# Optimization experiments

Hardware: AMD Instinct MI355X
Metric: run time of the kernel (lower is better)

The kernel has to match this reference:

```python
import jax, jax.numpy as jnp
import numpy as np

B, S, F = 32, 8, 4
N0, N1, N2 = 2048, 4096, 2048
H, OUT = 1024, 256
IN = N0 + N1 + N2  # 8192
SC_LAYERS = 2


def setup_inputs() -> dict:
    key = jax.random.key(0)
    ks = jax.random.split(key, 16)
    rn = jax.random.normal
    inp = {
        'xs0': rn(ks[0], (B, S, N0), jnp.float32),
        'xs1': rn(ks[1], (B, S, N1), jnp.float32),
        'xs2': rn(ks[2], (B, S, N2), jnp.float32),
        # dense Laplacians, scaled so L@x keeps unit-ish variance
        'L0': rn(ks[3], (N0, N0), jnp.float32) / np.sqrt(N0).astype(np.float32),
        'L1': rn(ks[4], (N1, N1), jnp.float32) / np.sqrt(N1).astype(np.float32),
        'L2': rn(ks[5], (N2, N2), jnp.float32) / np.sqrt(N2).astype(np.float32),
        # per-layer, per-filter diagonal weights (std=0.01 as in torch init)
        'Wc0': 0.01 * rn(ks[6], (SC_LAYERS, F, N0), jnp.float32),
        'Wc1': 0.01 * rn(ks[7], (SC_LAYERS, F, N1), jnp.float32),
        'Wc2': 0.01 * rn(ks[8], (SC_LAYERS, F, N2), jnp.float32),
        # MLP params (xavier-ish)
        'W_in': rn(ks[9], (IN, H), jnp.float32) / np.sqrt(IN).astype(np.float32),
        'b_in': jnp.zeros((H,), jnp.float32),
        'W_h': rn(ks[10], (H, H), jnp.float32) / np.sqrt(H).astype(np.float32),
        'b_h': jnp.zeros((H,), jnp.float32),
        'W_out': rn(ks[11], (H, OUT), jnp.float32) / np.sqrt(H).astype(np.float32),
        'b_out': jnp.zeros((OUT,), jnp.float32),
    }
    return inp


def _conv_stack(x, L, Wc):
    # x: [B, S, n]; L: [n, n]; Wc: [layers, F, n]
    for l in range(Wc.shape[0]):
        # batched Laplacian matmul: (L @ x_bs) for every (b, s)
        Lx = jnp.einsum('bsn,mn->bsm', x, L)  # [B, S, n]
        # diagonal filter scaling + activation + sum over filters (fused)
        x = jax.nn.relu(Lx[:, :, None, :] * Wc[l][None, None, :, :]).sum(axis=2)
    return x


def reference(xs0, xs1, xs2, L0, L1, L2, Wc0, Wc1, Wc2,
              W_in, b_in, W_h, b_h, W_out, b_out):
    h = jnp.concatenate([
        _conv_stack(xs0, L0, Wc0),
        _conv_stack(xs1, L1, Wc1),
        _conv_stack(xs2, L2, Wc2),
    ], axis=-1)                      # [B, S, IN]
    h = h.sum(axis=1)                # sum over sequence -> [B, IN]
    h = jax.nn.relu(h @ W_in + b_in)
    h = jax.nn.relu(h @ W_h + b_h)   # single hidden layer (nn_layers=2)
    return h @ W_out + b_out         # [B, OUT]
```

## Files before the change

kernel.cpp:

```cpp
#include <hip/hip_runtime.h>
#include <hip/hip_bf16.h>


#define B_    32
#define S_    8
#define BS_   256
#define F_    4
#define IN_   8192
#define H_    1024
#define OUT_  256

#define L_TOT  25165824LL
#define LOFF1  4194304LL
#define LOFF2  20971520LL

typedef __attribute__((ext_vector_type(8)))  short bf16x8;
typedef __attribute__((ext_vector_type(4)))  short short4v;
typedef __attribute__((ext_vector_type(16))) float f32x16;

typedef const __attribute__((address_space(1))) void* gas_ptr;
typedef __attribute__((address_space(3))) void* las_ptr;

__device__ __forceinline__ void gload16(const void* g, void* s) {
    __builtin_amdgcn_global_load_lds((gas_ptr)g, (las_ptr)s, 16, 0, 0);
}

__device__ __forceinline__ unsigned short rne_bf16(float f) {
    unsigned int u = __builtin_bit_cast(unsigned int, f);
    u += 0x7FFFu + ((u >> 16) & 1u);
    return (unsigned short)(u >> 16);
}

__global__ void k_prep(const float* __restrict__ Wc0, const float* __restrict__ Wc1,
                       const float* __restrict__ Wc2, float* __restrict__ PM) {
    int idx = blockIdx.x * 256 + threadIdx.x;
    if (idx >= 2 * IN_) return;
    int l = idx / IN_, n = idx % IN_;
    const float* Wc; int nb, j;
    if (n < 2048)      { Wc = Wc0; nb = 2048; j = n;        }
    else if (n < 6144) { Wc = Wc1; nb = 4096; j = n - 2048; }
    else               { Wc = Wc2; nb = 2048; j = n - 6144; }
    float p = 0.f, m = 0.f;
    #pragma unroll
    for (int f = 0; f < F_; ++f) {
        float w = Wc[(l * F_ + f) * nb + j];
        p += fmaxf(w, 0.f);
        m += fmaxf(-w, 0.f);
    }
    PM[(l * 2 + 0) * IN_ + n] = p;
    PM[(l * 2 + 1) * IN_ + n] = m;
}

__global__ void k_cvtL(const float* __restrict__ L0, const float* __restrict__ L1,
                       const float* __restrict__ L2, unsigned short* __restrict__ Lb) {
    const int gid = blockIdx.x * 256 + threadIdx.x;
    #pragma unroll 4
    for (int it = 0; it < 12; ++it) {
        long long e = ((long long)it * 524288 + gid) * 4;
        const float* src; long long off;
        if (e < LOFF1)      { src = L0; off = 0; }
        else if (e < LOFF2) { src = L1; off = LOFF1; }
        else                { src = L2; off = LOFF2; }
        float4 v = *(const float4*)(src + (e - off));
        short4v o;
        o.x = (short)rne_bf16(v.x); o.y = (short)rne_bf16(v.y);
        o.z = (short)rne_bf16(v.z); o.w = (short)rne_bf16(v.w);
        *(short4v*)(Lb + e) = o;
    }
}

__global__ void k_splitX(const float* __restrict__ x0, const float* __restrict__ x1,
                         const float* __restrict__ x2,
                         unsigned short* __restrict__ Xhi, unsigned short* __restrict__ Xlo) {
    int e = (blockIdx.x * 256 + threadIdx.x) * 4;
    int m = e >> 13, c = e & 8191;
    const float* src; int n, c0;
    if (c < 2048)      { src = x0; n = 2048; c0 = c; }
    else if (c < 6144) { src = x1; n = 4096; c0 = c - 2048; }
    else               { src = x2; n = 2048; c0 = c - 6144; }
    float4 v = *(const float4*)(src + (size_t)m * n + c0);
    float a[4] = {v.x, v.y, v.z, v.w};
    short hv[4], lv[4];
    #pragma unroll
    for (int i = 0; i < 4; ++i) {
        unsigned short hb = rne_bf16(a[i]);
        float hf = __builtin_bit_cast(float, (unsigned int)hb << 16);
        hv[i] = (short)hb;
        lv[i] = (short)rne_bf16(a[i] - hf);
    }
    short4v h = {hv[0], hv[1], hv[2], hv[3]};
    short4v l = {lv[0], lv[1], lv[2], lv[3]};
    *(short4v*)(Xhi + (size_t)m * IN_ + c) = h;
    *(short4v*)(Xlo + (size_t)m * IN_ + c) = l;
}

__global__ __launch_bounds__(256, 3) void k_gemm(
    const unsigned short* __restrict__ Xhi, const unsigned short* __restrict__ Xlo,
    const unsigned short* __restrict__ Lb,
    float* __restrict__ pf)
{
    __shared__ __attribute__((aligned(16))) unsigned short Ah[2][64 * 32];
    __shared__ __attribute__((aligned(16))) unsigned short Al[2][64 * 32];
    __shared__ __attribute__((aligned(16))) unsigned short Bs[2][128 * 32];

    const int bx = blockIdx.x;
    int n_, noff, mt, nt, sk; long long loff;
    if (bx < 128) {
        int u = bx; sk = u & 1; u >>= 1; mt = u >> 4; nt = u & 15;
        n_ = 2048; noff = 0; loff = 0;
    } else if (bx < 640) {
        int u = bx - 128; sk = u & 3; u >>= 2; mt = u >> 5; nt = u & 31;
        n_ = 4096; noff = 2048; loff = LOFF1;
    } else {
        int u = bx - 640; sk = u & 1; u >>= 1; mt = u >> 4; nt = u & 15;
        n_ = 2048; noff = 6144; loff = LOFF2;
    }
    const int k0 = sk << 10;

    const int tid = threadIdx.x, l = tid & 63, w = tid >> 6;

    const int sr  = 16 * w + (l >> 2);
    const int slg = (((l & 3) ^ ((l >> 3) & 3)) << 3);
    const unsigned short* gAh = Xhi + (size_t)(mt * 64 + sr) * IN_ + noff + k0 + slg;
    const unsigned short* gAl = Xlo + (size_t)(mt * 64 + sr) * IN_ + noff + k0 + slg;
    const unsigned short* gB0 = Lb + loff + (size_t)(nt * 128 + sr) * n_ + k0 + slg;
    const unsigned short* gB1 = Lb + loff + (size_t)(nt * 128 + 64 + sr) * n_ + k0 + slg;
    char* dAh[2] = {(char*)&Ah[0][0] + w * 1024, (char*)&Ah[1][0] + w * 1024};
    char* dAl[2] = {(char*)&Al[0][0] + w * 1024, (char*)&Al[1][0] + w * 1024};
    char* dB0[2] = {(char*)&Bs[0][0] + w * 1024, (char*)&Bs[1][0] + w * 1024};
    char* dB1[2] = {(char*)&Bs[0][0] + 4096 + w * 1024, (char*)&Bs[1][0] + 4096 + w * 1024};

    const int l31 = l & 31, lh = l >> 5;
    const int wm = w >> 1, wn = w & 1;
    const int ra  = (wm * 32 + l31) * 32;
    const int rb0 = (wn * 64 + l31) * 32;
    const int rb1 = rb0 + 32 * 32;
    const int swz = ((l31 >> 1) & 3);

    f32x16 acc0, acc1;
    #pragma unroll
    for (int r = 0; r < 16; ++r) { acc0[r] = 0.f; acc1[r] = 0.f; }

    gload16(gAh, dAh[0]); gload16(gAl, dAl[0]);
    gload16(gB0, dB0[0]); gload16(gB1, dB1[0]);
    __syncthreads();

    for (int it = 0; it < 32; ++it) {
        const int cur = it & 1, nxt = cur ^ 1;
        if (it + 1 < 32) {
            const int ko = (it + 1) * 32;
            gload16(gAh + ko, dAh[nxt]); gload16(gAl + ko, dAl[nxt]);
            gload16(gB0 + ko, dB0[nxt]); gload16(gB1 + ko, dB1[nxt]);
        }
        #pragma unroll
        for (int t = 0; t < 2; ++t) {
            const int sidx = (((2 * t + lh) ^ swz) << 3);
            bf16x8 fah = *(const bf16x8*)&Ah[cur][ra + sidx];
            bf16x8 fal = *(const bf16x8*)&Al[cur][ra + sidx];
            bf16x8 fb0 = *(const bf16x8*)&Bs[cur][rb0 + sidx];
            bf16x8 fb1 = *(const bf16x8*)&Bs[cur][rb1 + sidx];
            acc0 = __builtin_amdgcn_mfma_f32_32x32x16_bf16(fal, fb0, acc0, 0, 0, 0);
            acc0 = __builtin_amdgcn_mfma_f32_32x32x16_bf16(fah, fb0, acc0, 0, 0, 0);
            acc1 = __builtin_amdgcn_mfma_f32_32x32x16_bf16(fal, fb1, acc1, 0, 0, 0);
            acc1 = __builtin_amdgcn_mfma_f32_32x32x16_bf16(fah, fb1, acc1, 0, 0, 0);
        }
        __syncthreads();
    }

    const int colg = noff + nt * 128 + wn * 64 + l31;
    float* po = pf + ((size_t)sk * 256 + (size_t)mt * 64 + wm * 32 + 4 * lh) * IN_;
    #pragma unroll
    for (int r = 0; r < 16; ++r) {
        int row = (r & 3) + 8 * (r >> 2);
        po[(size_t)row * IN_ + colg]      = acc0[r];
        po[(size_t)row * IN_ + colg + 32] = acc1[r];
    }
}

__global__ void k_epi0(const float* __restrict__ pf,
                       const float* __restrict__ Pv, const float* __restrict__ Mv,
                       unsigned short* __restrict__ Yhi, unsigned short* __restrict__ Ylo) {
    int e = (blockIdx.x * 256 + threadIdx.x) * 4;
    int m = e >> 13, c = e & 8191;
    const int nsl = (c >= 2048 && c < 6144) ? 4 : 2;
    const float* p0 = pf + (size_t)m * IN_ + c;
    float vs[4] = {0.f, 0.f, 0.f, 0.f};
    for (int s = 0; s < nsl; ++s) {
        float4 v = *(const float4*)(p0 + (size_t)s * 256 * IN_);
        vs[0] += v.x; vs[1] += v.y; vs[2] += v.z; vs[3] += v.w;
    }
    float4 pv = *(const float4*)(Pv + c);
    float4 mv = *(const float4*)(Mv + c);
    float pa[4] = {pv.x, pv.y, pv.z, pv.w};
    float ma[4] = {mv.x, mv.y, mv.z, mv.w};
    short hv[4], lv[4];
    #pragma unroll
    for (int j = 0; j < 4; ++j) {
        float y = fmaxf(vs[j], 0.f) * pa[j] + fmaxf(-vs[j], 0.f) * ma[j];
        unsigned short hb = rne_bf16(y);
        float hf = __builtin_bit_cast(float, (unsigned int)hb << 16);
        hv[j] = (short)hb;
        lv[j] = (short)rne_bf16(y - hf);
    }
    short4v h = {hv[0], hv[1], hv[2], hv[3]};
    short4v lo = {lv[0], lv[1], lv[2], lv[3]};
    *(short4v*)(Yhi + (size_t)m * IN_ + c) = h;
    *(short4v*)(Ylo + (size_t)m * IN_ + c) = lo;
}

__global__ void k_epi1s(const float* __restrict__ pf,
                        const float* __restrict__ Pv, const float* __restrict__ Mv,
                        float* __restrict__ hsum) {
    int e = (blockIdx.x * 256 + threadIdx.x) * 4;
    int b = e >> 13, c = e & 8191;
    const int nsl = (c >= 2048 && c < 6144) ? 4 : 2;
    float4 pv = *(const float4*)(Pv + c);
    float4 mv = *(const float4*)(Mv + c);
    float pa[4] = {pv.x, pv.y, pv.z, pv.w};
    float ma[4] = {mv.x, mv.y, mv.z, mv.w};
    float hs[4] = {0.f, 0.f, 0.f, 0.f};
    for (int q = 0; q < 8; ++q) {
        const int m = b * 8 + q;
        const float* p0 = pf + (size_t)m * IN_ + c;
        float vs[4] = {0.f, 0.f, 0.f, 0.f};
        for (int s = 0; s < nsl; ++s) {
            float4 v = *(const float4*)(p0 + (size_t)s * 256 * IN_);
            vs[0] += v.x; vs[1] += v.y; vs[2] += v.z; vs[3] += v.w;
        }
        #pragma unroll
        for (int j = 0; j < 4; ++j)
            hs[j] += fmaxf(vs[j], 0.f) * pa[j] + fmaxf(-vs[j], 0.f) * ma[j];
    }
    *(float4*)(hsum + (size_t)b * IN_ + c) = *(float4*)hs;
}

template<int KC>
__global__ __launch_bounds__(256) void k_mlp3(
    const float* __restrict__ X, const float* __restrict__ W,
    float* __restrict__ P, int K, int H)
{
    __shared__ float Xs[32][KC];
    const int tid = threadIdx.x;
    const int lane = tid & 63;
    const int mg = tid >> 6;
    const int h = (blockIdx.x * 64 + lane) * 4;
    const int c = blockIdx.y, k0 = c * KC;

    for (int i = tid * 4; i < 32 * KC; i += 1024) {
        int m = i / KC, kk = i % KC;
        *(float4*)&Xs[m][kk] = *(const float4*)(X + (size_t)m * K + k0 + kk);
    }
    __syncthreads();

    float4 acc[8];
    #pragma unroll
    for (int m = 0; m < 8; ++m) acc[m] = {0.f, 0.f, 0.f, 0.f};

    const float* wp = W + (size_t)k0 * H + h;
    for (int kk = 0; kk < KC; kk += 4) {
        float4 w4[4];
        #pragma unroll
        for (int u = 0; u < 4; ++u)
            w4[u] = *(const float4*)(wp + (size_t)(kk + u) * H);
        #pragma unroll
        for (int m = 0; m < 8; ++m) {
            float4 xv = *(const float4*)&Xs[mg * 8 + m][kk];
            acc[m].x = fmaf(xv.x, w4[0].x, acc[m].x);
            acc[m].y = fmaf(xv.x, w4[0].y, acc[m].y);
            acc[m].z = fmaf(xv.x, w4[0].z, acc[m].z);
            acc[m].w = fmaf(xv.x, w4[0].w, acc[m].w);
            acc[m].x = fmaf(xv.y, w4[1].x, acc[m].x);
            acc[m].y = fmaf(xv.y, w4[1].y, acc[m].y);
            acc[m].z = fmaf(xv.y, w4[1].z, acc[m].z);
            acc[m].w = fmaf(xv.y, w4[1].w, acc[m].w);
            acc[m].x = fmaf(xv.z, w4[2].x, acc[m].x);
            acc[m].y = fmaf(xv.z, w4[2].y, acc[m].y);
            acc[m].z = fmaf(xv.z, w4[2].z, acc[m].z);
            acc[m].w = fmaf(xv.z, w4[2].w, acc[m].w);
            acc[m].x = fmaf(xv.w, w4[3].x, acc[m].x);
            acc[m].y = fmaf(xv.w, w4[3].y, acc[m].y);
            acc[m].z = fmaf(xv.w, w4[3].z, acc[m].z);
            acc[m].w = fmaf(xv.w, w4[3].w, acc[m].w);
        }
    }
    #pragma unroll
    for (int m = 0; m < 8; ++m)
        *(float4*)(P + ((size_t)c * 32 + mg * 8 + m) * H + h) = acc[m];
}

__global__ void k_reduce4(const float* __restrict__ P, const float* __restrict__ bias,
                          float* __restrict__ Y, int NC, int MH4, int H, int do_relu) {
    int idx = blockIdx.x * 256 + threadIdx.x;
    if (idx >= MH4) return;
    int h0 = (idx * 4) % H;
    float4 s = *(const float4*)(bias + h0);
    for (int c = 0; c < NC; ++c) {
        float4 v = *(const float4*)(P + (size_t)c * MH4 * 4 + (size_t)idx * 4);
        s.x += v.x; s.y += v.y; s.z += v.z; s.w += v.w;
    }
    if (do_relu) {
        s.x = fmaxf(s.x, 0.f); s.y = fmaxf(s.y, 0.f);
        s.z = fmaxf(s.z, 0.f); s.w = fmaxf(s.w, 0.f);
    }
    *(float4*)(Y + (size_t)idx * 4) = s;
}

extern "C" void kernel_launch(void* const* d_in, const int* in_sizes, int n_in,
                              void* d_out, int out_size, void* d_ws, size_t ws_size,
                              hipStream_t stream) {
    const float* xs0  = (const float*)d_in[0];
    const float* xs1  = (const float*)d_in[1];
    const float* xs2  = (const float*)d_in[2];
    const float* L0   = (const float*)d_in[3];
    const float* L1   = (const float*)d_in[4];
    const float* L2   = (const float*)d_in[5];
    const float* Wc0  = (const float*)d_in[6];
    const float* Wc1  = (const float*)d_in[7];
    const float* Wc2  = (const float*)d_in[8];
    const float* W_in = (const float*)d_in[9];
    const float* b_in = (const float*)d_in[10];
    const float* W_h  = (const float*)d_in[11];
    const float* b_h  = (const float*)d_in[12];
    const float* W_out= (const float*)d_in[13];
    const float* b_out= (const float*)d_in[14];

    char* w = (char*)d_ws;
    float*          PM  = (float*)w;          w += (size_t)4 * IN_ * 4;
    unsigned short* Lb  = (unsigned short*)w; w += (size_t)L_TOT * 2;
    unsigned short* Xhi = (unsigned short*)w; w += (size_t)BS_ * IN_ * 2;
    unsigned short* Xlo = (unsigned short*)w; w += (size_t)BS_ * IN_ * 2;
    unsigned short* Yhi = (unsigned short*)w; w += (size_t)BS_ * IN_ * 2;
    unsigned short* Ylo = (unsigned short*)w; w += (size_t)BS_ * IN_ * 2;
    float*          pf  = (float*)w;          w += (size_t)4 * BS_ * IN_ * 4;
    float*          hsum= (float*)w;          w += (size_t)32 * IN_ * 4;
    float*          p1  = pf;
    float*          h1  = (float*)w;          w += (size_t)32 * H_ * 4;
    float*          p2  = (float*)w;          w += (size_t)32 * 32 * H_ * 4;
    float*          h2  = (float*)w;          w += (size_t)32 * H_ * 4;
    float*          p3  = (float*)w;          w += (size_t)32 * 32 * OUT_ * 4;

    k_prep<<<64, 256, 0, stream>>>(Wc0, Wc1, Wc2, PM);
    k_cvtL<<<2048, 256, 0, stream>>>(L0, L1, L2, Lb);
    k_splitX<<<2048, 256, 0, stream>>>(xs0, xs1, xs2, Xhi, Xlo);

    k_gemm<<<768, 256, 0, stream>>>(Xhi, Xlo, Lb, pf);
    k_epi0<<<2048, 256, 0, stream>>>(pf, PM + 0 * IN_, PM + 1 * IN_, Yhi, Ylo);
    k_gemm<<<768, 256, 0, stream>>>(Yhi, Ylo, Lb, pf);
    k_epi1s<<<256, 256, 0, stream>>>(pf, PM + 2 * IN_, PM + 3 * IN_, hsum);

    {
        dim3 g(4, 128);
        k_mlp3<64><<<g, 256, 0, stream>>>(hsum, W_in, p1, IN_, H_);
        k_reduce4<<<32, 256, 0, stream>>>(p1, b_in, h1, 128, 8192, H_, 1);
    }
    {
        dim3 g(4, 32);
        k_mlp3<32><<<g, 256, 0, stream>>>(h1, W_h, p2, H_, H_);
        k_reduce4<<<32, 256, 0, stream>>>(p2, b_h, h2, 32, 8192, H_, 1);
    }
    {
        dim3 g(1, 32);
        k_mlp3<32><<<g, 256, 0, stream>>>(h2, W_out, p3, H_, OUT_);
        k_reduce4<<<8, 256, 0, stream>>>(p3, b_out, (float*)d_out, 32, 2048, OUT_, 0);
    }
}
```

Before: 211.9 us.

## Fuse preprocessing kernels and triple-buffer GEMM loads with one barrier per step

Merges the three preprocessing kernels (Wc folding, L bf16 conversion, X hi/lo split) into one launch and widens them to 8 elements per access. In the GEMM main loop, the LDS double buffer becomes a three-stage ring with two tiles prefetched ahead. The loop waits on vmcnt and uses a single barrier per iteration instead of two __syncthreads. This aims to cut launch overhead and hide global-to-LDS latency better, at the cost of more LDS per block, which may lower occupancy.

```diff
diff --git a/kernel.cpp b/kernel.cpp
--- a/kernel.cpp
+++ b/kernel.cpp
@@ -16,6 +16,7 @@
 
 typedef __attribute__((ext_vector_type(8)))  short bf16x8;
 typedef __attribute__((ext_vector_type(4)))  short short4v;
+typedef __attribute__((ext_vector_type(8)))  short short8v;
 typedef __attribute__((ext_vector_type(16))) float f32x16;
 
 typedef const __attribute__((address_space(1))) void* gas_ptr;
@@ -31,67 +32,80 @@
     return (unsigned short)(u >> 16);
 }
 
-__global__ void k_prep(const float* __restrict__ Wc0, const float* __restrict__ Wc1,
-                       const float* __restrict__ Wc2, float* __restrict__ PM) {
-    int idx = blockIdx.x * 256 + threadIdx.x;
-    if (idx >= 2 * IN_) return;
-    int l = idx / IN_, n = idx % IN_;
-    const float* Wc; int nb, j;
-    if (n < 2048)      { Wc = Wc0; nb = 2048; j = n;        }
-    else if (n < 6144) { Wc = Wc1; nb = 4096; j = n - 2048; }
-    else               { Wc = Wc2; nb = 2048; j = n - 6144; }
-    float p = 0.f, m = 0.f;
-    #pragma unroll
-    for (int f = 0; f < F_; ++f) {
-        float w = Wc[(l * F_ + f) * nb + j];
-        p += fmaxf(w, 0.f);
-        m += fmaxf(-w, 0.f);
-    }
-    PM[(l * 2 + 0) * IN_ + n] = p;
-    PM[(l * 2 + 1) * IN_ + n] = m;
-}
-
-__global__ void k_cvtL(const float* __restrict__ L0, const float* __restrict__ L1,
-                       const float* __restrict__ L2, unsigned short* __restrict__ Lb) {
-    const int gid = blockIdx.x * 256 + threadIdx.x;
-    #pragma unroll 4
-    for (int it = 0; it < 12; ++it) {
-        long long e = ((long long)it * 524288 + gid) * 4;
-        const float* src; long long off;
-        if (e < LOFF1)      { src = L0; off = 0; }
-        else if (e < LOFF2) { src = L1; off = LOFF1; }
-        else                { src = L2; off = LOFF2; }
-        float4 v = *(const float4*)(src + (e - off));
-        short4v o;
-        o.x = (short)rne_bf16(v.x); o.y = (short)rne_bf16(v.y);
-        o.z = (short)rne_bf16(v.z); o.w = (short)rne_bf16(v.w);
-        *(short4v*)(Lb + e) = o;
-    }
-}
-
-__global__ void k_splitX(const float* __restrict__ x0, const float* __restrict__ x1,
-                         const float* __restrict__ x2,
-                         unsigned short* __restrict__ Xhi, unsigned short* __restrict__ Xlo) {
-    int e = (blockIdx.x * 256 + threadIdx.x) * 4;
-    int m = e >> 13, c = e & 8191;
-    const float* src; int n, c0;
-    if (c < 2048)      { src = x0; n = 2048; c0 = c; }
-    else if (c < 6144) { src = x1; n = 4096; c0 = c - 2048; }
-    else               { src = x2; n = 2048; c0 = c - 6144; }
-    float4 v = *(const float4*)(src + (size_t)m * n + c0);
-    float a[4] = {v.x, v.y, v.z, v.w};
-    short hv[4], lv[4];
-    #pragma unroll
-    for (int i = 0; i < 4; ++i) {
-        unsigned short hb = rne_bf16(a[i]);
-        float hf = __builtin_bit_cast(float, (unsigned int)hb << 16);
-        hv[i] = (short)hb;
-        lv[i] = (short)rne_bf16(a[i] - hf);
-    }
-    short4v h = {hv[0], hv[1], hv[2], hv[3]};
-    short4v l = {lv[0], lv[1], lv[2], lv[3]};
-    *(short4v*)(Xhi + (size_t)m * IN_ + c) = h;
-    *(short4v*)(Xlo + (size_t)m * IN_ + c) = l;
+__global__ void k_pre(const float* __restrict__ L0, const float* __restrict__ L1,
+                      const float* __restrict__ L2, unsigned short* __restrict__ Lb,
+                      const float* __restrict__ x0, const float* __restrict__ x1,
+                      const float* __restrict__ x2,
+                      unsigned short* __restrict__ Xhi, unsigned short* __restrict__ Xlo,
+                      const float* __restrict__ Wc0, const float* __restrict__ Wc1,
+                      const float* __restrict__ Wc2, float* __restrict__ PM)
+{
+    const int bx = blockIdx.x, tid = threadIdx.x;
+    if (bx < 3072) {
+        const long long base = (long long)bx * 8192 + tid * 8;
+        #pragma unroll
+        for (int u = 0; u < 4; ++u) {
+            long long e = base + (long long)u * 2048;
+            const float* src; long long off;
+            if (e < LOFF1)      { src = L0; off = 0; }
+            else if (e < LOFF2) { src = L1; off = LOFF1; }
+            else                { src = L2; off = LOFF2; }
+            const float* p = src + (e - off);
+            float4 a = *(const float4*)(p);
+            float4 b = *(const float4*)(p + 4);
+            short8v o;
+            o[0] = (short)rne_bf16(a.x); o[1] = (short)rne_bf16(a.y);
+            o[2] = (short)rne_bf16(a.z); o[3] = (short)rne_bf16(a.w);
+            o[4] = (short)rne_bf16(b.x); o[5] = (short)rne_bf16(b.y);
+            o[6] = (short)rne_bf16(b.z); o[7] = (short)rne_bf16(b.w);
+            *(short8v*)(Lb + e) = o;
+        }
+    } else if (bx < 3584) {
+        const int base = (bx - 3072) * 4096 + tid * 8;
+        #pragma unroll
+        for (int u = 0; u < 2; ++u) {
+            int e = base + u * 2048;
+            int m = e >> 13, c = e & 8191;
+            const float* src; int n, c0;
+            if (c < 2048)      { src = x0; n = 2048; c0 = c; }
+            else if (c < 6144) { src = x1; n = 4096; c0 = c - 2048; }
+            else               { src = x2; n = 2048; c0 = c - 6144; }
+            const float* p = src + (size_t)m * n + c0;
+            float4 a = *(const float4*)(p);
+            float4 b = *(const float4*)(p + 4);
+            float v[8] = {a.x, a.y, a.z, a.w, b.x, b.y, b.z, b.w};
+            short8v h, l;
+            #pragma unroll
+            for (int i = 0; i < 8; ++i) {
+                unsigned short hb = rne_bf16(v[i]);
+                float hf = __builtin_bit_cast(float, (unsigned int)hb << 16);
+                h[i] = (short)hb;
+                l[i] = (short)rne_bf16(v[i] - hf);
+            }
+            *(short8v*)(Xhi + (size_t)m * IN_ + c) = h;
+            *(short8v*)(Xlo + (size_t)m * IN_ + c) = l;
+        }
+    } else {
+        const int base = (bx - 3584) * 2048 + tid * 8;
+        #pragma unroll
+        for (int i = 0; i < 8; ++i) {
+            int idx = base + i;
+            int l = idx / IN_, n = idx % IN_;
+            const float* Wc; int nb, j;
+            if (n < 2048)      { Wc = Wc0; nb = 2048; j = n;        }
+            else if (n < 6144) { Wc = Wc1; nb = 4096; j = n - 2048; }
+            else               { Wc = Wc2; nb = 2048; j = n - 6144; }
+            float p = 0.f, m = 0.f;
+            #pragma unroll
+            for (int f = 0; f < F_; ++f) {
+                float w = Wc[(l * F_ + f) * nb + j];
+                p += fmaxf(w, 0.f);
+                m += fmaxf(-w, 0.f);
+            }
+            PM[(l * 2 + 0) * IN_ + n] = p;
+            PM[(l * 2 + 1) * IN_ + n] = m;
+        }
+    }
 }
 
 __global__ __launch_bounds__(256, 3) void k_gemm(
@@ -99,9 +113,9 @@
     const unsigned short* __restrict__ Lb,
     float* __restrict__ pf)
 {
-    __shared__ __attribute__((aligned(16))) unsigned short Ah[2][64 * 32];
-    __shared__ __attribute__((aligned(16))) unsigned short Al[2][64 * 32];
-    __shared__ __attribute__((aligned(16))) unsigned short Bs[2][128 * 32];
+    __shared__ __attribute__((aligned(16))) unsigned short Ah[3][64 * 32];
+    __shared__ __attribute__((aligned(16))) unsigned short Al[3][64 * 32];
+    __shared__ __attribute__((aligned(16))) unsigned short Bs[3][128 * 32];
 
     const int bx = blockIdx.x;
     int n_, noff, mt, nt, sk; long long loff;
@@ -125,10 +139,6 @@
     const unsigned short* gAl = Xlo + (size_t)(mt * 64 + sr) * IN_ + noff + k0 + slg;
     const unsigned short* gB0 = Lb + loff + (size_t)(nt * 128 + sr) * n_ + k0 + slg;
     const unsigned short* gB1 = Lb + loff + (size_t)(nt * 128 + 64 + sr) * n_ + k0 + slg;
-    char* dAh[2] = {(char*)&Ah[0][0] + w * 1024, (char*)&Ah[1][0] + w * 1024};
-    char* dAl[2] = {(char*)&Al[0][0] + w * 1024, (char*)&Al[1][0] + w * 1024};
-    char* dB0[2] = {(char*)&Bs[0][0] + w * 1024, (char*)&Bs[1][0] + w * 1024};
-    char* dB1[2] = {(char*)&Bs[0][0] + 4096 + w * 1024, (char*)&Bs[1][0] + 4096 + w * 1024};
 
     const int l31 = l & 31, lh = l >> 5;
     const int wm = w >> 1, wn = w & 1;
@@ -141,17 +151,31 @@
     #pragma unroll
     for (int r = 0; r < 16; ++r) { acc0[r] = 0.f; acc1[r] = 0.f; }
 
-    gload16(gAh, dAh[0]); gload16(gAl, dAl[0]);
-    gload16(gB0, dB0[0]); gload16(gB1, dB1[0]);
-    __syncthreads();
+    #define STAGE(slot, ko)                                                     \
+        do {                                                                    \
+            gload16(gAh + (ko), (char*)&Ah[slot][0] + w * 1024);                \
+            gload16(gAl + (ko), (char*)&Al[slot][0] + w * 1024);                \
+            gload16(gB0 + (ko), (char*)&Bs[slot][0] + w * 1024);                \
+            gload16(gB1 + (ko), (char*)&Bs[slot][0] + 4096 + w * 1024);         \
+        } while (0)
+
+    STAGE(0, 0);
+    STAGE(1, 32);
 
     for (int it = 0; it < 32; ++it) {
-        const int cur = it & 1, nxt = cur ^ 1;
-        if (it + 1 < 32) {
-            const int ko = (it + 1) * 32;
-            gload16(gAh + ko, dAh[nxt]); gload16(gAl + ko, dAl[nxt]);
-            gload16(gB0 + ko, dB0[nxt]); gload16(gB1 + ko, dB1[nxt]);
-        }
+        if (it + 1 < 32) asm volatile("s_waitcnt vmcnt(4)" ::: "memory");
+        else             asm volatile("s_waitcnt vmcnt(0)" ::: "memory");
+        __builtin_amdgcn_s_barrier();
+        asm volatile("" ::: "memory");
+
+        if (it + 2 < 32) {
+            const int slot = (it + 2) % 3;
+            const int ko = (it + 2) * 32;
+            STAGE(slot, ko);
+        }
+        __builtin_amdgcn_sched_barrier(0);
+
+        const int cur = it % 3;
         #pragma unroll
         for (int t = 0; t < 2; ++t) {
             const int sidx = (((2 * t + lh) ^ swz) << 3);
@@ -164,8 +188,9 @@
             acc1 = __builtin_amdgcn_mfma_f32_32x32x16_bf16(fal, fb1, acc1, 0, 0, 0);
             acc1 = __builtin_amdgcn_mfma_f32_32x32x16_bf16(fah, fb1, acc1, 0, 0, 0);
         }
-        __syncthreads();
-    }
+        asm volatile("" ::: "memory");
+    }
+    #undef STAGE
 
     const int colg = noff + nt * 128 + wn * 64 + l31;
     float* po = pf + ((size_t)sk * 256 + (size_t)mt * 64 + wm * 32 + 4 * lh) * IN_;
@@ -339,9 +364,8 @@
     float*          h2  = (float*)w;          w += (size_t)32 * H_ * 4;
     float*          p3  = (float*)w;          w += (size_t)32 * 32 * OUT_ * 4;
 
-    k_prep<<<64, 256, 0, stream>>>(Wc0, Wc1, Wc2, PM);
-    k_cvtL<<<2048, 256, 0, stream>>>(L0, L1, L2, Lb);
-    k_splitX<<<2048, 256, 0, stream>>>(xs0, xs1, xs2, Xhi, Xlo);
+    k_pre<<<3592, 256, 0, stream>>>(L0, L1, L2, Lb, xs0, xs1, xs2, Xhi, Xlo,
+                                    Wc0, Wc1, Wc2, PM);
 
     k_gemm<<<768, 256, 0, stream>>>(Xhi, Xlo, Lb, pf);
     k_epi0<<<2048, 256, 0, stream>>>(pf, PM + 0 * IN_, PM + 1 * IN_, Yhi, Ylo);
```

New measurement: 199.2 us. -6.0%, faster.
